# Kernel optimization log

Measured on AMD Instinct MI355X. Metric: run time of the kernel, lower is better.

## Reference

```python
import jax, jax.numpy as jnp
import numpy as np

LN_EPS = 1e-3  # keras LayerNormalization default epsilon


def setup_inputs() -> dict:
    key = jax.random.key(0)
    ks = jax.random.split(key, 6)
    B, S, D, H, K = 4, 4096, 1024, 16, 64
    scale = 1.0 / np.sqrt(D)
    return {
        "x": jax.random.normal(ks[0], (B, S, D), jnp.float32),
        "Wq": jax.random.normal(ks[1], (D, H, K), jnp.float32) * scale,
        "bq": jnp.zeros((H, K), jnp.float32),
        "Wk": jax.random.normal(ks[2], (D, H, K), jnp.float32) * scale,
        "bk": jnp.zeros((H, K), jnp.float32),
        "Wv": jax.random.normal(ks[3], (D, H, K), jnp.float32) * scale,
        "bv": jnp.zeros((H, K), jnp.float32),
        "Wo": jax.random.normal(ks[4], (H, K, D), jnp.float32) * scale,
        "bo": jnp.zeros((D,), jnp.float32),
        "gamma": jnp.ones((D,), jnp.float32),
        "beta": jnp.zeros((D,), jnp.float32),
        "num_window": 8,
    }


def reference(x, Wq, bq, Wk, bk, Wv, bv, Wo, bo, gamma, beta, num_window):
    B, S, D = x.shape
    H, K = Wq.shape[1], Wq.shape[2]
    Sw = S // num_window
    # Block-diagonal (windowed) attention: reshape seq into windows instead of a Python loop.
    xw = x.reshape(B, num_window, Sw, D)  # [B, W, Sw, D]
    q = jnp.einsum('bwsd,dhk->bwshk', xw, Wq) + bq
    k = jnp.einsum('bwsd,dhk->bwshk', xw, Wk) + bk
    v = jnp.einsum('bwsd,dhk->bwshk', xw, Wv) + bv
    scores = jnp.einsum('bwqhk,bwshk->bwhqs', q, k) / jnp.sqrt(jnp.asarray(K, x.dtype))
    attn = jax.nn.softmax(scores, axis=-1)  # [B, W, H, Sw, Sw]
    ctx = jnp.einsum('bwhqs,bwshk->bwqhk', attn, v)
    attn_out = (jnp.einsum('bwqhk,hkd->bwqd', ctx, Wo) + bo).reshape(B, S, D)
    # residual + layernorm (keras eps=1e-3)
    y = x + attn_out
    mu = jnp.mean(y, axis=-1, keepdims=True)
    var = jnp.mean(jnp.square(y - mu), axis=-1, keepdims=True)
    return (y - mu) * jax.lax.rsqrt(var + LN_EPS) * gamma + beta
```

## Files before the change

kernel.cpp:

```cpp
#include <hip/hip_runtime.h>

typedef __bf16 bf16_t;
typedef __bf16 bf16x4 __attribute__((ext_vector_type(4)));
typedef __bf16 bf16x8 __attribute__((ext_vector_type(8)));
typedef float f32x4 __attribute__((ext_vector_type(4)));

#define MFMA16(a, b, c) __builtin_amdgcn_mfma_f32_16x16x32_bf16((a), (b), (c), 0, 0, 0)

#define FENCE asm volatile("" ::: "memory")
#define BAR()                        \
  do {                               \
    FENCE;                           \
    __builtin_amdgcn_s_barrier();    \
    FENCE;                           \
  } while (0)
#define WAITLGKM(n) asm volatile("s_waitcnt lgkmcnt(" #n ")" ::: "memory")

__device__ __forceinline__ void gl_lds16(const bf16_t* g, bf16_t* l) {
  __builtin_amdgcn_global_load_lds(
      (const __attribute__((address_space(1))) void*)g,
      (__attribute__((address_space(3))) void*)l, 16, 0, 0);
}

__global__ __launch_bounds__(256) void cast_x_kernel(const float* __restrict__ x,
                                                     bf16_t* __restrict__ xb) {
  size_t i = (size_t)blockIdx.x * 256 + threadIdx.x;
  float4 v = ((const float4*)x)[i];
  bf16x4 o = {(bf16_t)v.x, (bf16_t)v.y, (bf16_t)v.z, (bf16_t)v.w};
  ((bf16x4*)xb)[i] = o;
}

__global__ __launch_bounds__(256) void transpose_w_kernel(
    const float* __restrict__ Wq, const float* __restrict__ Wk,
    const float* __restrict__ Wv, const float* __restrict__ Wo,
    bf16_t* __restrict__ Wt, bf16_t* __restrict__ WoT) {
  __shared__ bf16_t T[64 * 68];
  const int z = blockIdx.z;
  const float* src = (z == 0) ? Wq : (z == 1) ? Wk : (z == 2) ? Wv : Wo;
  bf16_t* dst = (z < 3) ? (Wt + (size_t)z * 1024 * 1024) : WoT;
  const int tr = blockIdx.y * 64;
  const int tc = blockIdx.x * 64;
  const int tid = threadIdx.x;
#pragma unroll
  for (int it = 0; it < 4; ++it) {
    int t = tid + it * 256;
    int row = t >> 4, c4 = t & 15;
    float4 v = *(const float4*)&src[(size_t)(tr + row) * 1024 + tc + c4 * 4];
    bf16x4 o = {(bf16_t)v.x, (bf16_t)v.y, (bf16_t)v.z, (bf16_t)v.w};
    *(bf16x4*)&T[row * 68 + c4 * 4] = o;
  }
  __syncthreads();
#pragma unroll
  for (int it = 0; it < 2; ++it) {
    int t = tid + it * 256;
    int n = t >> 3, d8 = t & 7;
    bf16x8 o;
#pragma unroll
    for (int j = 0; j < 8; ++j) o[j] = T[(d8 * 8 + j) * 68 + n];
    *(bf16x8*)&dst[(size_t)(tc + n) * 1024 + tr + d8 * 8] = o;
  }
}


__device__ __forceinline__ void stage_half(const bf16_t* __restrict__ g,
                                           bf16_t* l, const int tid) {
#pragma unroll
  for (int j = 0; j < 2; ++j) {
    int idx = j * 512 + tid;
    int row = idx >> 3;
    int c = (idx & 7) ^ (row & 7);
    gl_lds16(g + (size_t)row * 1024 + c * 8, l + idx * 8);
  }
}

__device__ __forceinline__ void tile_step(const int t, bf16_t* const buf,
                                          bf16_t* const nbuf,
                                          const bf16_t* __restrict__ Ab,
                                          const bf16_t* __restrict__ Bb,
                                          f32x4 (&acc)[8][4], const int tid) {
  const int l15 = tid & 15, quad = (tid >> 4) & 3;
  const int wv = tid >> 6, wm = wv >> 2, wn = wv & 3;
  const int sx = l15 & 7;
  const int brow0 = (wn & 1) * 64;
  const bf16_t* const Ar = buf + wm * 8192;
  const bf16_t* const Br = buf + (2 + (wn >> 1)) * 8192;

  bf16x8 af[4][2], bfr[4][2];

#pragma unroll
  for (int nf = 0; nf < 2; ++nf)
#pragma unroll
    for (int ks = 0; ks < 2; ++ks)
      bfr[nf][ks] = *(const bf16x8*)&Br[(brow0 + nf * 16 + l15) * 64 +
                                        (((ks * 4 + quad) ^ sx) << 3)];
  FENCE;
#pragma unroll
  for (int mf = 0; mf < 2; ++mf)
#pragma unroll
    for (int ks = 0; ks < 2; ++ks)
      af[mf][ks] = *(const bf16x8*)&Ar[(mf * 16 + l15) * 64 +
                                       (((ks * 4 + quad) ^ sx) << 3)];
  FENCE;
#pragma unroll
  for (int mf = 2; mf < 4; ++mf)
#pragma unroll
    for (int ks = 0; ks < 2; ++ks)
      af[mf][ks] = *(const bf16x8*)&Ar[(mf * 16 + l15) * 64 +
                                       (((ks * 4 + quad) ^ sx) << 3)];
  FENCE;
  if (t + 1 < 16) stage_half(Bb + 128 * 1024 + (t + 1) * 64, nbuf + 3 * 8192, tid);
  BAR();
  WAITLGKM(4);
  __builtin_amdgcn_s_setprio(1);
#pragma unroll
  for (int ks = 0; ks < 2; ++ks)
#pragma unroll
    for (int mf = 0; mf < 2; ++mf)
#pragma unroll
      for (int nf = 0; nf < 2; ++nf)
        acc[mf][nf] = MFMA16(af[mf][ks], bfr[nf][ks], acc[mf][nf]);
  __builtin_amdgcn_s_setprio(0);
  WAITLGKM(0);
  __builtin_amdgcn_s_setprio(1);
#pragma unroll
  for (int ks = 0; ks < 2; ++ks)
#pragma unroll
    for (int mf = 2; mf < 4; ++mf)
#pragma unroll
      for (int nf = 0; nf < 2; ++nf)
        acc[mf][nf] = MFMA16(af[mf][ks], bfr[nf][ks], acc[mf][nf]);
  __builtin_amdgcn_s_setprio(0);
  BAR();

#pragma unroll
  for (int nf = 2; nf < 4; ++nf)
#pragma unroll
    for (int ks = 0; ks < 2; ++ks)
      bfr[nf][ks] = *(const bf16x8*)&Br[(brow0 + nf * 16 + l15) * 64 +
                                        (((ks * 4 + quad) ^ sx) << 3)];
  FENCE;
  if (t + 1 < 16) stage_half(Ab + 128 * 1024 + (t + 1) * 64, nbuf + 1 * 8192, tid);
  BAR();
  WAITLGKM(0);
  __builtin_amdgcn_s_setprio(1);
#pragma unroll
  for (int ks = 0; ks < 2; ++ks)
#pragma unroll
    for (int mf = 0; mf < 4; ++mf)
#pragma unroll
      for (int nf = 2; nf < 4; ++nf)
        acc[mf][nf] = MFMA16(af[mf][ks], bfr[nf][ks], acc[mf][nf]);
  __builtin_amdgcn_s_setprio(0);
  BAR();

#pragma unroll
  for (int mf = 0; mf < 2; ++mf)
#pragma unroll
    for (int ks = 0; ks < 2; ++ks)
      af[mf][ks] = *(const bf16x8*)&Ar[((mf + 4) * 16 + l15) * 64 +
                                       (((ks * 4 + quad) ^ sx) << 3)];
  FENCE;
#pragma unroll
  for (int mf = 2; mf < 4; ++mf)
#pragma unroll
    for (int ks = 0; ks < 2; ++ks)
      af[mf][ks] = *(const bf16x8*)&Ar[((mf + 4) * 16 + l15) * 64 +
                                       (((ks * 4 + quad) ^ sx) << 3)];
  FENCE;
  if (t + 2 < 16) stage_half(Bb + (t + 2) * 64, buf + 2 * 8192, tid);
  BAR();
  WAITLGKM(4);
  __builtin_amdgcn_s_setprio(1);
#pragma unroll
  for (int ks = 0; ks < 2; ++ks)
#pragma unroll
    for (int mf = 0; mf < 2; ++mf)
#pragma unroll
      for (int nf = 2; nf < 4; ++nf)
        acc[mf + 4][nf] = MFMA16(af[mf][ks], bfr[nf][ks], acc[mf + 4][nf]);
  __builtin_amdgcn_s_setprio(0);
  WAITLGKM(0);
  __builtin_amdgcn_s_setprio(1);
#pragma unroll
  for (int ks = 0; ks < 2; ++ks)
#pragma unroll
    for (int mf = 2; mf < 4; ++mf)
#pragma unroll
      for (int nf = 2; nf < 4; ++nf)
        acc[mf + 4][nf] = MFMA16(af[mf][ks], bfr[nf][ks], acc[mf + 4][nf]);
  __builtin_amdgcn_s_setprio(0);
  BAR();

  if (t + 2 < 16) stage_half(Ab + (t + 2) * 64, buf + 0 * 8192, tid);
  BAR();
  __builtin_amdgcn_s_setprio(1);
#pragma unroll
  for (int ks = 0; ks < 2; ++ks)
#pragma unroll
    for (int mf = 0; mf < 4; ++mf)
#pragma unroll
      for (int nf = 0; nf < 2; ++nf)
        acc[mf + 4][nf] = MFMA16(af[mf][ks], bfr[nf][ks], acc[mf + 4][nf]);
  __builtin_amdgcn_s_setprio(0);
  if (t < 14)
    asm volatile("s_waitcnt vmcnt(4)" ::: "memory");
  else
    asm volatile("s_waitcnt vmcnt(0)" ::: "memory");
  BAR();
}

__device__ __forceinline__ void gemm256_main(const bf16_t* __restrict__ Ab,
                                             const bf16_t* __restrict__ Bb,
                                             bf16_t* lds, f32x4 (&acc)[8][4],
                                             const int tid) {
  stage_half(Bb, lds + 2 * 8192, tid);
  stage_half(Ab, lds + 0 * 8192, tid);
  stage_half(Bb + 128 * 1024, lds + 3 * 8192, tid);
  stage_half(Ab + 128 * 1024, lds + 1 * 8192, tid);
  stage_half(Bb + 64, lds + 6 * 8192, tid);
  stage_half(Ab + 64, lds + 4 * 8192, tid);
  asm volatile("s_waitcnt vmcnt(4)" ::: "memory");
  BAR();

  for (int t = 0; t < 16; t += 2) {
    tile_step(t, lds, lds + 32768, Ab, Bb, acc, tid);
    tile_step(t + 1, lds + 32768, lds, Ab, Bb, acc, tid);
  }
}

__global__ __launch_bounds__(512) void gemm_qkv_kernel(
    const bf16_t* __restrict__ A, const bf16_t* __restrict__ Bt,
    const float* __restrict__ bq, const float* __restrict__ bk,
    const float* __restrict__ bv, bf16_t* __restrict__ C) {
  __shared__ bf16_t lds[2 * 4 * 8192];
  const int tid = threadIdx.x;
  const int lin = blockIdx.x;
  const int swz = (lin & 7) * 96 + (lin >> 3);
  const int bm = swz / 12, bn = swz - bm * 12;

  f32x4 acc[8][4];
#pragma unroll
  for (int i = 0; i < 8; ++i)
#pragma unroll
    for (int j = 0; j < 4; ++j)
#pragma unroll
      for (int e = 0; e < 4; ++e) acc[i][j][e] = 0.f;

  gemm256_main(A + (size_t)(bm * 256) * 1024, Bt + (size_t)(bn * 256) * 1024,
               lds, acc, tid);

  const int l15 = tid & 15, quad = (tid >> 4) & 3;
  const int wv = tid >> 6, wm = wv >> 2, wn = wv & 3;
  const int col0 = bn * 256 + wn * 64;
  const int rbase = bm * 256 + wm * 128;
  float* R = (float*)(lds + wv * 8192);

  float wbias[4], wscale[4];
#pragma unroll
  for (int nf = 0; nf < 4; ++nf) {
    int col = col0 + nf * 16 + l15;
    if (col < 1024) {
      wbias[nf] = bq[col];
      wscale[nf] = 0.125f;
    } else if (col < 2048) {
      wbias[nf] = bk[col - 1024];
      wscale[nf] = 1.f;
    } else {
      wbias[nf] = bv[col - 2048];
      wscale[nf] = 1.f;
    }
  }
#pragma unroll
  for (int p = 0; p < 4; ++p) {
#pragma unroll
    for (int mfi = 0; mfi < 2; ++mfi) {
#pragma unroll
      for (int nf = 0; nf < 4; ++nf)
#pragma unroll
        for (int r = 0; r < 4; ++r)
          R[(mfi * 16 + quad * 4 + r) * 68 + nf * 16 + l15] =
              (acc[p * 2 + mfi][nf][r] + wbias[nf]) * wscale[nf];
    }
    WAITLGKM(0);
#pragma unroll
    for (int i = 0; i < 8; ++i) {
      const int lr = i * 4 + quad;
      f32x4 vv = *(const f32x4*)&R[lr * 68 + l15 * 4];
      bf16x4 o = {(bf16_t)vv[0], (bf16_t)vv[1], (bf16_t)vv[2], (bf16_t)vv[3]};
      int row = rbase + p * 32 + lr;
      *(bf16x4*)&C[(size_t)row * 3072 + col0 + l15 * 4] = o;
    }
    WAITLGKM(0);
  }
}

__global__ __launch_bounds__(256) void attn_kernel(
    const bf16_t* __restrict__ QKV, bf16_t* __restrict__ Ctx) {
  __shared__ bf16_t Ks[64 * 64];
  __shared__ bf16_t Vs[64 * 64];
  __shared__ bf16_t Pb[4][16 * 64];

  const int tid = threadIdx.x;
  const int wv = tid >> 6, quad = (tid >> 4) & 3, l15 = tid & 15;
  const int hid = blockIdx.x, qb = blockIdx.y;
  const int b = hid >> 7, w = (hid >> 4) & 7, h = hid & 15;
  const int rowW = b * 4096 + w * 512;
  const int qbase = qb * 128 + wv * 32;

  bf16x8 qf[2][2];
#pragma unroll
  for (int qt = 0; qt < 2; ++qt) {
    int rowQ = rowW + qbase + qt * 16 + l15;
#pragma unroll
    for (int kh = 0; kh < 2; ++kh)
      qf[qt][kh] = *(const bf16x8*)&QKV[(size_t)rowQ * 3072 + h * 64 + kh * 32 + quad * 8];
  }

  const bf16_t* Kb = QKV + (size_t)rowW * 3072 + 1024 + h * 64;
  const bf16_t* Vg = QKV + (size_t)rowW * 3072 + 2048 + h * 64;

  float lp[2] = {0.f, 0.f};
  f32x4 Oa[2][4];
  f32x4 zero = {0.f, 0.f, 0.f, 0.f};
#pragma unroll
  for (int qt = 0; qt < 2; ++qt)
#pragma unroll
    for (int dt = 0; dt < 4; ++dt) Oa[qt][dt] = zero;

  const int vrow = tid >> 2;
  const int vseg = tid & 3;

  for (int kt = 0; kt < 8; ++kt) {
#pragma unroll
    for (int i = 0; i < 2; ++i) {
      int t = tid + i * 256;
      int row = t >> 3;
      int g = (t & 7) ^ (row & 7);
      gl_lds16(Kb + (size_t)(kt * 64 + row) * 3072 + g * 8, &Ks[t * 8]);
    }
    {
      const bf16_t* src = Vg + (size_t)(kt * 64 + vrow) * 3072 + vseg * 16;
      bf16x8 v0 = *(const bf16x8*)&src[0];
      bf16x8 v1 = *(const bf16x8*)&src[8];
      int sg = vrow >> 3, sr = vrow & 7;
#pragma unroll
      for (int j = 0; j < 8; ++j) {
        int d0 = vseg * 16 + j;
        Vs[d0 * 64 + ((sg ^ (d0 & 7)) << 3) + sr] = v0[j];
        int d1 = vseg * 16 + 8 + j;
        Vs[d1 * 64 + ((sg ^ (d1 & 7)) << 3) + sr] = v1[j];
      }
    }
    __syncthreads();

    bf16x8 kf[4][2], vf[2][4];
#pragma unroll
    for (int jt = 0; jt < 4; ++jt) {
      int key = jt * 16 + l15;
#pragma unroll
      for (int kh = 0; kh < 2; ++kh)
        kf[jt][kh] = *(const bf16x8*)&Ks[key * 64 + (((kh * 4 + quad) ^ (key & 7)) << 3)];
    }
#pragma unroll
    for (int kh = 0; kh < 2; ++kh)
#pragma unroll
      for (int dt = 0; dt < 4; ++dt) {
        int d = dt * 16 + l15;
        vf[kh][dt] = *(const bf16x8*)&Vs[d * 64 + (((kh * 4 + quad) ^ (d & 7)) << 3)];
      }

#pragma unroll
    for (int qt = 0; qt < 2; ++qt) {
      f32x4 st[4];
#pragma unroll
      for (int jt = 0; jt < 4; ++jt) {
        f32x4 a = zero;
#pragma unroll
        for (int kh = 0; kh < 2; ++kh) a = MFMA16(kf[jt][kh], qf[qt][kh], a);
        st[jt] = a;
      }
      float ls = 0.f;
#pragma unroll
      for (int jt = 0; jt < 4; ++jt)
#pragma unroll
        for (int r = 0; r < 4; ++r) {
          float p = __expf(st[jt][r]);
          st[jt][r] = p;
          ls += p;
        }
      lp[qt] += ls;
#pragma unroll
      for (int jt = 0; jt < 4; ++jt) {
        bf16x4 pk = {(bf16_t)st[jt][0], (bf16_t)st[jt][1],
                     (bf16_t)st[jt][2], (bf16_t)st[jt][3]};
        int gs = (jt * 2 + (quad >> 1)) ^ (l15 & 7);
        *(bf16x4*)&Pb[wv][l15 * 64 + gs * 8 + (quad & 1) * 4] = pk;
      }
#pragma unroll
      for (int kh = 0; kh < 2; ++kh) {
        bf16x8 pf = *(const bf16x8*)&Pb[wv][l15 * 64 + (((kh * 4 + quad) ^ (l15 & 7)) << 3)];
#pragma unroll
        for (int dt = 0; dt < 4; ++dt) Oa[qt][dt] = MFMA16(pf, vf[kh][dt], Oa[qt][dt]);
      }
    }
    __syncthreads();
  }

#pragma unroll
  for (int qt = 0; qt < 2; ++qt) {
    float t = lp[qt];
    t += __shfl_xor(t, 16, 64);
    t += __shfl_xor(t, 32, 64);
    float inv_l = 1.0f / t;
    float inv[4];
#pragma unroll
    for (int r = 0; r < 4; ++r) inv[r] = __shfl(inv_l, quad * 4 + r, 64);
#pragma unroll
    for (int dt = 0; dt < 4; ++dt)
#pragma unroll
      for (int r = 0; r < 4; ++r) {
        int orow = rowW + qbase + qt * 16 + quad * 4 + r;
        Ctx[(size_t)orow * 1024 + h * 64 + dt * 16 + l15] = (bf16_t)(Oa[qt][dt][r] * inv[r]);
      }
  }
}

__global__ __launch_bounds__(512) void gemm_proj_kernel(
    const bf16_t* __restrict__ A, const bf16_t* __restrict__ Bt,
    const float* __restrict__ bo, const float* __restrict__ x,
    bf16_t* __restrict__ Yb) {
  __shared__ bf16_t lds[2 * 4 * 8192];
  const int tid = threadIdx.x;
  const int lin = blockIdx.x;
  const int swz = (lin & 7) * 32 + (lin >> 3);
  const int bm = swz >> 2, bn = swz & 3;

  f32x4 acc[8][4];
#pragma unroll
  for (int i = 0; i < 8; ++i)
#pragma unroll
    for (int j = 0; j < 4; ++j)
#pragma unroll
      for (int e = 0; e < 4; ++e) acc[i][j][e] = 0.f;

  gemm256_main(A + (size_t)(bm * 256) * 1024, Bt + (size_t)(bn * 256) * 1024,
               lds, acc, tid);

  const int l15 = tid & 15, quad = (tid >> 4) & 3;
  const int wv = tid >> 6, wm = wv >> 2, wn = wv & 3;
  const int col0 = bn * 256 + wn * 64;
  const int rbase = bm * 256 + wm * 128;
  float* R = (float*)(lds + wv * 8192);
  const int colg = col0 + l15 * 4;
  const float4 bo4 = *(const float4*)&bo[colg];

#pragma unroll
  for (int p = 0; p < 4; ++p) {
#pragma unroll
    for (int mfi = 0; mfi < 2; ++mfi) {
#pragma unroll
      for (int nf = 0; nf < 4; ++nf)
#pragma unroll
        for (int r = 0; r < 4; ++r)
          R[(mfi * 16 + quad * 4 + r) * 68 + nf * 16 + l15] = acc[p * 2 + mfi][nf][r];
    }
    WAITLGKM(0);
#pragma unroll
    for (int i = 0; i < 8; ++i) {
      const int lr = i * 4 + quad;
      int row = rbase + p * 32 + lr;
      f32x4 vv = *(const f32x4*)&R[lr * 68 + l15 * 4];
      float4 xv = *(const float4*)&x[(size_t)row * 1024 + colg];
      bf16x4 o = {(bf16_t)(vv[0] + bo4.x + xv.x), (bf16_t)(vv[1] + bo4.y + xv.y),
                  (bf16_t)(vv[2] + bo4.z + xv.z), (bf16_t)(vv[3] + bo4.w + xv.w)};
      *(bf16x4*)&Yb[(size_t)row * 1024 + colg] = o;
    }
    WAITLGKM(0);
  }
}

__global__ __launch_bounds__(256) void ln_kernel(const bf16_t* __restrict__ Yb,
                                                 float* __restrict__ Y,
                                                 const float* __restrict__ gamma,
                                                 const float* __restrict__ beta) {
  const int row = blockIdx.x, tid = threadIdx.x;
  bf16x4 yb = ((const bf16x4*)(Yb + (size_t)row * 1024))[tid];
  float y0 = (float)yb[0], y1 = (float)yb[1], y2 = (float)yb[2], y3 = (float)yb[3];
  float s = y0 + y1 + y2 + y3;
  float s2 = y0 * y0 + y1 * y1 + y2 * y2 + y3 * y3;
#pragma unroll
  for (int off = 1; off < 64; off <<= 1) {
    s += __shfl_xor(s, off, 64);
    s2 += __shfl_xor(s2, off, 64);
  }
  __shared__ float red[8];
  int wv = tid >> 6;
  if ((tid & 63) == 0) {
    red[wv] = s;
    red[4 + wv] = s2;
  }
  __syncthreads();
  s = red[0] + red[1] + red[2] + red[3];
  s2 = red[4] + red[5] + red[6] + red[7];
  float mean = s * (1.0f / 1024.0f);
  float var = s2 * (1.0f / 1024.0f) - mean * mean;
  float rs = rsqrtf(var + 1e-3f);
  float4 g = ((const float4*)gamma)[tid];
  float4 bb = ((const float4*)beta)[tid];
  float4 o;
  o.x = (y0 - mean) * rs * g.x + bb.x;
  o.y = (y1 - mean) * rs * g.y + bb.y;
  o.z = (y2 - mean) * rs * g.z + bb.z;
  o.w = (y3 - mean) * rs * g.w + bb.w;
  ((float4*)(Y + (size_t)row * 1024))[tid] = o;
}

extern "C" void kernel_launch(void* const* d_in, const int* in_sizes, int n_in,
                              void* d_out, int out_size, void* d_ws, size_t ws_size,
                              hipStream_t stream) {
  const float* x = (const float*)d_in[0];
  const float* Wq = (const float*)d_in[1];
  const float* bq = (const float*)d_in[2];
  const float* Wk = (const float*)d_in[3];
  const float* bk = (const float*)d_in[4];
  const float* Wv = (const float*)d_in[5];
  const float* bv = (const float*)d_in[6];
  const float* Wo = (const float*)d_in[7];
  const float* bo = (const float*)d_in[8];
  const float* gamma = (const float*)d_in[9];
  const float* beta = (const float*)d_in[10];
  float* Y = (float*)d_out;

  char* ws = (char*)d_ws;
  bf16_t* xb = (bf16_t*)(ws);
  bf16_t* Wt = (bf16_t*)(ws + 33554432);
  bf16_t* WoT = (bf16_t*)(ws + 39845888);
  bf16_t* QKVb = (bf16_t*)(ws + 41943040);
  bf16_t* Ctx = (bf16_t*)(ws + 142606336);
  bf16_t* Yb = (bf16_t*)(ws + 176160768);

  cast_x_kernel<<<16384, 256, 0, stream>>>(x, xb);
  transpose_w_kernel<<<dim3(16, 16, 4), 256, 0, stream>>>(Wq, Wk, Wv, Wo, Wt, WoT);
  gemm_qkv_kernel<<<768, 512, 0, stream>>>(xb, Wt, bq, bk, bv, QKVb);
  attn_kernel<<<dim3(512, 4), 256, 0, stream>>>(QKVb, Ctx);
  gemm_proj_kernel<<<256, 512, 0, stream>>>(Ctx, WoT, bo, x, Yb);
  ln_kernel<<<16384, 256, 0, stream>>>(Yb, Y, gamma, beta);
}
```

Before: 373.1 us.

## Load full A/B fragments upfront per tile step and cut barriers

Restructures the GEMM tile step so each wave loads all eight A fragments and all four B fragment groups from LDS at the start, rather than reloading A halves mid-step. Both next-tile staging loads are issued together, and several barriers between MFMA phases are removed, with lgkmcnt waits ordering the compute. The aim is less barrier synchronisation and LDS reload traffic, so MFMAs overlap better with global-to-LDS copies. The cost is roughly double the A-fragment registers, which may reduce occupancy or spill. Dropping barriers before overwriting LDS buffers risks races.

Result: slower. 415.6 us (+11.4%).

```diff
diff --git a/kernel.cpp b/kernel.cpp
--- a/kernel.cpp
+++ b/kernel.cpp
@@ -85,7 +85,7 @@
   const bf16_t* const Ar = buf + wm * 8192;
   const bf16_t* const Br = buf + (2 + (wn >> 1)) * 8192;
 
-  bf16x8 af[4][2], bfr[4][2];
+  bf16x8 af[8][2], bfr[4][2];
 
 #pragma unroll
   for (int nf = 0; nf < 2; ++nf)
@@ -95,53 +95,44 @@
                                         (((ks * 4 + quad) ^ sx) << 3)];
   FENCE;
 #pragma unroll
-  for (int mf = 0; mf < 2; ++mf)
+  for (int mf = 0; mf < 4; ++mf)
 #pragma unroll
     for (int ks = 0; ks < 2; ++ks)
       af[mf][ks] = *(const bf16x8*)&Ar[(mf * 16 + l15) * 64 +
                                        (((ks * 4 + quad) ^ sx) << 3)];
   FENCE;
 #pragma unroll
-  for (int mf = 2; mf < 4; ++mf)
+  for (int nf = 2; nf < 4; ++nf)
+#pragma unroll
+    for (int ks = 0; ks < 2; ++ks)
+      bfr[nf][ks] = *(const bf16x8*)&Br[(brow0 + nf * 16 + l15) * 64 +
+                                        (((ks * 4 + quad) ^ sx) << 3)];
+  FENCE;
+#pragma unroll
+  for (int mf = 4; mf < 8; ++mf)
 #pragma unroll
     for (int ks = 0; ks < 2; ++ks)
       af[mf][ks] = *(const bf16x8*)&Ar[(mf * 16 + l15) * 64 +
                                        (((ks * 4 + quad) ^ sx) << 3)];
   FENCE;
-  if (t + 1 < 16) stage_half(Bb + 128 * 1024 + (t + 1) * 64, nbuf + 3 * 8192, tid);
+  if (t + 1 < 16) {
+    stage_half(Bb + 128 * 1024 + (t + 1) * 64, nbuf + 3 * 8192, tid);
+    stage_half(Ab + 128 * 1024 + (t + 1) * 64, nbuf + 1 * 8192, tid);
+  }
   BAR();
-  WAITLGKM(4);
+
+  WAITLGKM(12);
   __builtin_amdgcn_s_setprio(1);
 #pragma unroll
   for (int ks = 0; ks < 2; ++ks)
 #pragma unroll
-    for (int mf = 0; mf < 2; ++mf)
+    for (int mf = 0; mf < 4; ++mf)
 #pragma unroll
       for (int nf = 0; nf < 2; ++nf)
         acc[mf][nf] = MFMA16(af[mf][ks], bfr[nf][ks], acc[mf][nf]);
   __builtin_amdgcn_s_setprio(0);
-  WAITLGKM(0);
-  __builtin_amdgcn_s_setprio(1);
-#pragma unroll
-  for (int ks = 0; ks < 2; ++ks)
-#pragma unroll
-    for (int mf = 2; mf < 4; ++mf)
-#pragma unroll
-      for (int nf = 0; nf < 2; ++nf)
-        acc[mf][nf] = MFMA16(af[mf][ks], bfr[nf][ks], acc[mf][nf]);
-  __builtin_amdgcn_s_setprio(0);
-  BAR();
-
-#pragma unroll
-  for (int nf = 2; nf < 4; ++nf)
-#pragma unroll
-    for (int ks = 0; ks < 2; ++ks)
-      bfr[nf][ks] = *(const bf16x8*)&Br[(brow0 + nf * 16 + l15) * 64 +
-                                        (((ks * 4 + quad) ^ sx) << 3)];
-  FENCE;
-  if (t + 1 < 16) stage_half(Ab + 128 * 1024 + (t + 1) * 64, nbuf + 1 * 8192, tid);
-  BAR();
-  WAITLGKM(0);
+
+  WAITLGKM(8);
   __builtin_amdgcn_s_setprio(1);
 #pragma unroll
   for (int ks = 0; ks < 2; ++ks)
@@ -153,54 +144,28 @@
   __builtin_amdgcn_s_setprio(0);
   BAR();
 
-#pragma unroll
-  for (int mf = 0; mf < 2; ++mf)
-#pragma unroll
-    for (int ks = 0; ks < 2; ++ks)
-      af[mf][ks] = *(const bf16x8*)&Ar[((mf + 4) * 16 + l15) * 64 +
-                                       (((ks * 4 + quad) ^ sx) << 3)];
-  FENCE;
-#pragma unroll
-  for (int mf = 2; mf < 4; ++mf)
-#pragma unroll
-    for (int ks = 0; ks < 2; ++ks)
-      af[mf][ks] = *(const bf16x8*)&Ar[((mf + 4) * 16 + l15) * 64 +
-                                       (((ks * 4 + quad) ^ sx) << 3)];
-  FENCE;
   if (t + 2 < 16) stage_half(Bb + (t + 2) * 64, buf + 2 * 8192, tid);
-  BAR();
-  WAITLGKM(4);
-  __builtin_amdgcn_s_setprio(1);
-#pragma unroll
-  for (int ks = 0; ks < 2; ++ks)
-#pragma unroll
-    for (int mf = 0; mf < 2; ++mf)
-#pragma unroll
-      for (int nf = 2; nf < 4; ++nf)
-        acc[mf + 4][nf] = MFMA16(af[mf][ks], bfr[nf][ks], acc[mf + 4][nf]);
-  __builtin_amdgcn_s_setprio(0);
   WAITLGKM(0);
   __builtin_amdgcn_s_setprio(1);
 #pragma unroll
   for (int ks = 0; ks < 2; ++ks)
 #pragma unroll
-    for (int mf = 2; mf < 4; ++mf)
+    for (int mf = 4; mf < 8; ++mf)
 #pragma unroll
       for (int nf = 2; nf < 4; ++nf)
-        acc[mf + 4][nf] = MFMA16(af[mf][ks], bfr[nf][ks], acc[mf + 4][nf]);
+        acc[mf][nf] = MFMA16(af[mf][ks], bfr[nf][ks], acc[mf][nf]);
   __builtin_amdgcn_s_setprio(0);
   BAR();
 
   if (t + 2 < 16) stage_half(Ab + (t + 2) * 64, buf + 0 * 8192, tid);
-  BAR();
   __builtin_amdgcn_s_setprio(1);
 #pragma unroll
   for (int ks = 0; ks < 2; ++ks)
 #pragma unroll
-    for (int mf = 0; mf < 4; ++mf)
+    for (int mf = 4; mf < 8; ++mf)
 #pragma unroll
       for (int nf = 0; nf < 2; ++nf)
-        acc[mf + 4][nf] = MFMA16(af[mf][ks], bfr[nf][ks], acc[mf + 4][nf]);
+        acc[mf][nf] = MFMA16(af[mf][ks], bfr[nf][ks], acc[mf][nf]);
   __builtin_amdgcn_s_setprio(0);
   if (t < 14)
     asm volatile("s_waitcnt vmcnt(4)" ::: "memory");
```

## Double-buffer K/V tiles in attention and drop redundant GEMM barriers

Applied to the files above, without the earlier changes.

The attention kernel now double-buffers K and V in shared memory, prefetching the next key tile and holding the next V tile in registers while the current tile is computed. This removes one barrier per iteration of load latency. The shared GEMM tile step merges its B and A stages, cutting several block barriers, and both GEMM kernels gain a launch bound of two blocks per CU. Removing barriers risks LDS overwrite races if the wait counts do not cover the in-flight async copies, and the occupancy hint may force register spills.

Measured after the change: 365.9 us. About the same (-1.9%).

```diff
diff --git a/kernel.cpp b/kernel.cpp
--- a/kernel.cpp
+++ b/kernel.cpp
@@ -108,9 +108,19 @@
       af[mf][ks] = *(const bf16x8*)&Ar[(mf * 16 + l15) * 64 +
                                        (((ks * 4 + quad) ^ sx) << 3)];
   FENCE;
-  if (t + 1 < 16) stage_half(Bb + 128 * 1024 + (t + 1) * 64, nbuf + 3 * 8192, tid);
-  BAR();
-  WAITLGKM(4);
+#pragma unroll
+  for (int nf = 2; nf < 4; ++nf)
+#pragma unroll
+    for (int ks = 0; ks < 2; ++ks)
+      bfr[nf][ks] = *(const bf16x8*)&Br[(brow0 + nf * 16 + l15) * 64 +
+                                        (((ks * 4 + quad) ^ sx) << 3)];
+  FENCE;
+  if (t + 1 < 16) {
+    stage_half(Bb + 128 * 1024 + (t + 1) * 64, nbuf + 3 * 8192, tid);
+    stage_half(Ab + 128 * 1024 + (t + 1) * 64, nbuf + 1 * 8192, tid);
+  }
+
+  WAITLGKM(8);
   __builtin_amdgcn_s_setprio(1);
 #pragma unroll
   for (int ks = 0; ks < 2; ++ks)
@@ -120,7 +130,8 @@
       for (int nf = 0; nf < 2; ++nf)
         acc[mf][nf] = MFMA16(af[mf][ks], bfr[nf][ks], acc[mf][nf]);
   __builtin_amdgcn_s_setprio(0);
-  WAITLGKM(0);
+
+  WAITLGKM(4);
   __builtin_amdgcn_s_setprio(1);
 #pragma unroll
   for (int ks = 0; ks < 2; ++ks)
@@ -130,17 +141,7 @@
       for (int nf = 0; nf < 2; ++nf)
         acc[mf][nf] = MFMA16(af[mf][ks], bfr[nf][ks], acc[mf][nf]);
   __builtin_amdgcn_s_setprio(0);
-  BAR();
-
-#pragma unroll
-  for (int nf = 2; nf < 4; ++nf)
-#pragma unroll
-    for (int ks = 0; ks < 2; ++ks)
-      bfr[nf][ks] = *(const bf16x8*)&Br[(brow0 + nf * 16 + l15) * 64 +
-                                        (((ks * 4 + quad) ^ sx) << 3)];
-  FENCE;
-  if (t + 1 < 16) stage_half(Ab + 128 * 1024 + (t + 1) * 64, nbuf + 1 * 8192, tid);
-  BAR();
+
   WAITLGKM(0);
   __builtin_amdgcn_s_setprio(1);
 #pragma unroll
@@ -153,6 +154,7 @@
   __builtin_amdgcn_s_setprio(0);
   BAR();
 
+  if (t + 2 < 16) stage_half(Bb + (t + 2) * 64, buf + 2 * 8192, tid);
 #pragma unroll
   for (int mf = 0; mf < 2; ++mf)
 #pragma unroll
@@ -167,8 +169,6 @@
       af[mf][ks] = *(const bf16x8*)&Ar[((mf + 4) * 16 + l15) * 64 +
                                        (((ks * 4 + quad) ^ sx) << 3)];
   FENCE;
-  if (t + 2 < 16) stage_half(Bb + (t + 2) * 64, buf + 2 * 8192, tid);
-  BAR();
   WAITLGKM(4);
   __builtin_amdgcn_s_setprio(1);
 #pragma unroll
@@ -192,7 +192,6 @@
   BAR();
 
   if (t + 2 < 16) stage_half(Ab + (t + 2) * 64, buf + 0 * 8192, tid);
-  BAR();
   __builtin_amdgcn_s_setprio(1);
 #pragma unroll
   for (int ks = 0; ks < 2; ++ks)
@@ -228,7 +227,7 @@
   }
 }
 
-__global__ __launch_bounds__(512) void gemm_qkv_kernel(
+__global__ __launch_bounds__(512, 2) void gemm_qkv_kernel(
     const bf16_t* __restrict__ A, const bf16_t* __restrict__ Bt,
     const float* __restrict__ bq, const float* __restrict__ bk,
     const float* __restrict__ bv, bf16_t* __restrict__ C) {
@@ -296,8 +295,8 @@
 
 __global__ __launch_bounds__(256) void attn_kernel(
     const bf16_t* __restrict__ QKV, bf16_t* __restrict__ Ctx) {
-  __shared__ bf16_t Ks[64 * 64];
-  __shared__ bf16_t Vs[64 * 64];
+  __shared__ bf16_t Ks[2][64 * 64];
+  __shared__ bf16_t Vs[2][64 * 64];
   __shared__ bf16_t Pb[4][16 * 64];
 
   const int tid = threadIdx.x;
@@ -329,29 +328,53 @@
 
   const int vrow = tid >> 2;
   const int vseg = tid & 3;
-
+  const int sg = vrow >> 3, sr = vrow & 7;
+
+  bf16x8 vr0, vr1;
+  {
+    const bf16_t* src = Vg + (size_t)vrow * 3072 + vseg * 16;
+    vr0 = *(const bf16x8*)&src[0];
+    vr1 = *(const bf16x8*)&src[8];
+  }
+  FENCE;
+#pragma unroll
+  for (int i = 0; i < 2; ++i) {
+    int t = tid + i * 256;
+    int row = t >> 3;
+    int g = (t & 7) ^ (row & 7);
+    gl_lds16(Kb + (size_t)row * 3072 + g * 8, &Ks[0][t * 8]);
+  }
+  FENCE;
+
+#pragma unroll 2
   for (int kt = 0; kt < 8; ++kt) {
-#pragma unroll
-    for (int i = 0; i < 2; ++i) {
-      int t = tid + i * 256;
-      int row = t >> 3;
-      int g = (t & 7) ^ (row & 7);
-      gl_lds16(Kb + (size_t)(kt * 64 + row) * 3072 + g * 8, &Ks[t * 8]);
-    }
-    {
-      const bf16_t* src = Vg + (size_t)(kt * 64 + vrow) * 3072 + vseg * 16;
-      bf16x8 v0 = *(const bf16x8*)&src[0];
-      bf16x8 v1 = *(const bf16x8*)&src[8];
-      int sg = vrow >> 3, sr = vrow & 7;
-#pragma unroll
-      for (int j = 0; j < 8; ++j) {
-        int d0 = vseg * 16 + j;
-        Vs[d0 * 64 + ((sg ^ (d0 & 7)) << 3) + sr] = v0[j];
-        int d1 = vseg * 16 + 8 + j;
-        Vs[d1 * 64 + ((sg ^ (d1 & 7)) << 3) + sr] = v1[j];
+    const int cb = kt & 1;
+    bf16x8 vn0 = vr0, vn1 = vr1;
+    if (kt < 7) {
+      const bf16_t* src = Vg + (size_t)((kt + 1) * 64 + vrow) * 3072 + vseg * 16;
+      vn0 = *(const bf16x8*)&src[0];
+      vn1 = *(const bf16x8*)&src[8];
+      FENCE;
+#pragma unroll
+      for (int i = 0; i < 2; ++i) {
+        int t = tid + i * 256;
+        int row = t >> 3;
+        int g = (t & 7) ^ (row & 7);
+        gl_lds16(Kb + (size_t)((kt + 1) * 64 + row) * 3072 + g * 8, &Ks[cb ^ 1][t * 8]);
       }
-    }
-    __syncthreads();
+      asm volatile("s_waitcnt vmcnt(4)" ::: "memory");
+    } else {
+      asm volatile("s_waitcnt vmcnt(0)" ::: "memory");
+    }
+#pragma unroll
+    for (int j = 0; j < 8; ++j) {
+      int d0 = vseg * 16 + j;
+      Vs[cb][d0 * 64 + ((sg ^ (d0 & 7)) << 3) + sr] = vr0[j];
+      int d1 = vseg * 16 + 8 + j;
+      Vs[cb][d1 * 64 + ((sg ^ (d1 & 7)) << 3) + sr] = vr1[j];
+    }
+    WAITLGKM(0);
+    BAR();
 
     bf16x8 kf[4][2], vf[2][4];
 #pragma unroll
@@ -359,14 +382,14 @@
       int key = jt * 16 + l15;
 #pragma unroll
       for (int kh = 0; kh < 2; ++kh)
-        kf[jt][kh] = *(const bf16x8*)&Ks[key * 64 + (((kh * 4 + quad) ^ (key & 7)) << 3)];
+        kf[jt][kh] = *(const bf16x8*)&Ks[cb][key * 64 + (((kh * 4 + quad) ^ (key & 7)) << 3)];
     }
 #pragma unroll
     for (int kh = 0; kh < 2; ++kh)
 #pragma unroll
       for (int dt = 0; dt < 4; ++dt) {
         int d = dt * 16 + l15;
-        vf[kh][dt] = *(const bf16x8*)&Vs[d * 64 + (((kh * 4 + quad) ^ (d & 7)) << 3)];
+        vf[kh][dt] = *(const bf16x8*)&Vs[cb][d * 64 + (((kh * 4 + quad) ^ (d & 7)) << 3)];
       }
 
 #pragma unroll
@@ -403,7 +426,10 @@
         for (int dt = 0; dt < 4; ++dt) Oa[qt][dt] = MFMA16(pf, vf[kh][dt], Oa[qt][dt]);
       }
     }
-    __syncthreads();
+    WAITLGKM(0);
+    BAR();
+    vr0 = vn0;
+    vr1 = vn1;
   }
 
 #pragma unroll
@@ -425,7 +451,7 @@
   }
 }
 
-__global__ __launch_bounds__(512) void gemm_proj_kernel(
+__global__ __launch_bounds__(512, 2) void gemm_proj_kernel(
     const bf16_t* __restrict__ A, const bf16_t* __restrict__ Bt,
     const float* __restrict__ bo, const float* __restrict__ x,
     bf16_t* __restrict__ Yb) {
```
